# Performance work log

Hardware: AMD Instinct MI355X
Metric: run time of the kernel (lower is better)

The kernel has to match this reference:

```python
import jax, jax.numpy as jnp
import numpy as np

T, D, I, E, K = 2048, 1024, 1024, 8, 2  # tokens, dim, moe_inter_dim, n_experts, top_k


def setup_inputs() -> dict:
    key = jax.random.key(0)
    ks = jax.random.split(key, 6)
    x = jax.random.normal(ks[0], (T, D), dtype=jnp.float32)
    token_mask = jnp.ones((T,), dtype=bool)
    weights = jax.random.uniform(ks[1], (T, K), dtype=jnp.float32)
    indices = jax.random.randint(ks[2], (T, K), 0, E, dtype=jnp.int32)
    scale = 0.02
    gate_projs = jax.random.normal(ks[3], (E, I, D), dtype=jnp.float32) * scale
    up_projs = jax.random.normal(ks[4], (E, I, D), dtype=jnp.float32) * scale
    down_projs = jax.random.normal(ks[5], (E, D, I), dtype=jnp.float32) * scale
    return {"x": x, "token_mask": token_mask, "weights": weights,
            "indices": indices, "gate_projs": gate_projs,
            "up_projs": up_projs, "down_projs": down_projs}


def reference(x, token_mask, weights, indices, gate_projs, up_projs, down_projs):
    # Combined routing weight per (token, expert): sum over top-k slots that
    # selected expert e, zeroed for masked-out tokens. Equivalent to the
    # torch gather -> swiglu -> weighted scatter_add loop.
    n_experts = gate_projs.shape[0]
    one_hot = (indices[..., None] == jnp.arange(n_experts)).astype(x.dtype)  # [T,K,E]
    w = jnp.einsum('tk,tke->te', weights, one_hot)                            # [T,E]
    w = w * token_mask.astype(x.dtype)[:, None]
    # Per-expert SwiGLU over all tokens, combined with routing weights.
    g = jnp.einsum('td,eid->eti', x, gate_projs)   # [E,T,I]
    u = jnp.einsum('td,eid->eti', x, up_projs)     # [E,T,I]
    h = jax.nn.silu(g) * u                          # [E,T,I]
    out = jnp.einsum('eti,edi->etd', h, down_projs)  # [E,T,D]
    y = jnp.einsum('etd,te->td', out, w)             # [T,D]
    return y
```

## Files before the change

### kernel.cpp

```cpp
#include <hip/hip_runtime.h>
#include <hip/hip_bf16.h>

#define T_TOK 2048
#define DDIM  1024
#define IDIM  1024
#define NEXP  8
#define TOPK  2
#define MAXROWS (T_TOK * TOPK)

#define BM 64
#define BN 64
#define BK 32
#define LDT 40
#define BUFSZ (64 * LDT)

typedef __attribute__((ext_vector_type(8))) short          s16x8;
typedef __attribute__((ext_vector_type(8))) unsigned short u16x8;
typedef __attribute__((ext_vector_type(4))) float          f32x4;

__device__ __forceinline__ unsigned short f2bf(float f) {
    unsigned int u = __builtin_bit_cast(unsigned int, f);
    unsigned int r = 0x7fffu + ((u >> 16) & 1u);
    return (unsigned short)((u + r) >> 16);
}

__device__ __forceinline__ u16x8 pack8(const float4& a, const float4& b) {
    u16x8 v;
    v[0] = f2bf(a.x); v[1] = f2bf(a.y); v[2] = f2bf(a.z); v[3] = f2bf(a.w);
    v[4] = f2bf(b.x); v[5] = f2bf(b.y); v[6] = f2bf(b.z); v[7] = f2bf(b.w);
    return v;
}

__global__ void route_kernel(const int* __restrict__ indices,
                             const float* __restrict__ weights,
                             const void* __restrict__ mask,
                             int* __restrict__ counts, int* __restrict__ offsets,
                             int* __restrict__ tok, float* __restrict__ wslot) {
    __shared__ int cnt[NEXP], offs[NEXP], cur[NEXP];
    __shared__ int is_u8;
    const int tid = threadIdx.x;
    const unsigned char* m8  = (const unsigned char*)mask;
    const int*           m32 = (const int*)mask;
    if (tid < NEXP) cnt[tid] = 0;
    if (tid == 0) is_u8 = 0;
    __syncthreads();
    int found = 0;
    for (int i = tid; i < T_TOK; i += blockDim.x)
        if ((i & 3) != 0 && m8[i] != 0) found = 1;
    if (found) atomicOr(&is_u8, 1);
    __syncthreads();
    const int u8mode = is_u8;
    for (int idx = tid; idx < MAXROWS; idx += blockDim.x) {
        int t = idx >> 1;
        int active = u8mode ? (m8[t] != 0) : (m32[t] != 0);
        if (active) atomicAdd(&cnt[indices[idx]], 1);
    }
    __syncthreads();
    if (tid == 0) {
        int run = 0;
        for (int e = 0; e < NEXP; ++e) { offs[e] = run; run += cnt[e]; }
    }
    __syncthreads();
    if (tid < NEXP) { counts[tid] = cnt[tid]; offsets[tid] = offs[tid]; cur[tid] = offs[tid]; }
    __syncthreads();
    for (int idx = tid; idx < MAXROWS; idx += blockDim.x) {
        int t = idx >> 1;
        int active = u8mode ? (m8[t] != 0) : (m32[t] != 0);
        if (active) {
            int e = indices[idx];
            int p = atomicAdd(&cur[e], 1);
            tok[p]   = t;
            wslot[p] = weights[idx];
        }
    }
}

__global__ __launch_bounds__(256) void cvt_x_kernel(const float* __restrict__ x,
                                                    unsigned short* __restrict__ xb) {
    int i = (blockIdx.x * 256 + threadIdx.x) * 8;
    float4 a = *reinterpret_cast<const float4*>(x + i);
    float4 b = *reinterpret_cast<const float4*>(x + i + 4);
    *reinterpret_cast<u16x8*>(xb + i) = pack8(a, b);
}

__global__ __launch_bounds__(256) void gemm1_kernel(
    const unsigned short* __restrict__ xb,
    const float* __restrict__ gate, const float* __restrict__ up,
    const int* __restrict__ counts, const int* __restrict__ offsets,
    const int* __restrict__ tok, unsigned short* __restrict__ hb) {
    const int e     = blockIdx.z;
    const int n_e   = counts[e];
    const int tileM = blockIdx.y;
    if (tileM * BM >= n_e) return;
    const int off = offsets[e];
    const int n0  = blockIdx.x * BN;

    __shared__ unsigned short lA[2 * BUFSZ];
    __shared__ unsigned short lG[2 * BUFSZ];
    __shared__ unsigned short lU[2 * BUFSZ];

    const int tid  = threadIdx.x;
    const int lane = tid & 63;
    const int wid  = tid >> 6;
    const int wm   = wid >> 1, wn = wid & 1;

    const int sr = tid >> 2, sseg = tid & 3;
    const int rowIdx = tileM * BM + sr;
    const int tIdx = (rowIdx < n_e) ? tok[off + rowIdx] : tok[off];
    const unsigned short* aSrc = xb + (size_t)tIdx * DDIM + sseg * 8;
    const float* gSrc = gate + ((size_t)e * IDIM + n0 + sr) * DDIM + sseg * 8;
    const float* uSrc = up   + ((size_t)e * IDIM + n0 + sr) * DDIM + sseg * 8;
    const int dstOff = sr * LDT + sseg * 8;

    f32x4 accg[2][2] = {};
    f32x4 accu[2][2] = {};

    const int fr  = lane & 15;
    const int fkb = (lane >> 4) * 8;

    uint4  av;
    float4 gv0, gv1, uv0, uv1;

    auto LOAD = [&](int k0) {
        av  = *reinterpret_cast<const uint4*>(aSrc + k0);
        gv0 = *reinterpret_cast<const float4*>(gSrc + k0);
        gv1 = *reinterpret_cast<const float4*>(gSrc + k0 + 4);
        uv0 = *reinterpret_cast<const float4*>(uSrc + k0);
        uv1 = *reinterpret_cast<const float4*>(uSrc + k0 + 4);
    };

    auto STORE = [&](int b) {
        *reinterpret_cast<uint4*>(&lA[b * BUFSZ + dstOff]) = av;
        *reinterpret_cast<u16x8*>(&lG[b * BUFSZ + dstOff]) = pack8(gv0, gv1);
        *reinterpret_cast<u16x8*>(&lU[b * BUFSZ + dstOff]) = pack8(uv0, uv1);
    };

    auto COMPUTE = [&](int b) {
        const unsigned short* pA = &lA[b * BUFSZ];
        const unsigned short* pG = &lG[b * BUFSZ];
        const unsigned short* pU = &lU[b * BUFSZ];
        s16x8 a0  = *reinterpret_cast<const s16x8*>(pA + (wm * 32 + fr) * LDT + fkb);
        s16x8 a1  = *reinterpret_cast<const s16x8*>(pA + (wm * 32 + 16 + fr) * LDT + fkb);
        s16x8 bg0 = *reinterpret_cast<const s16x8*>(pG + (wn * 32 + fr) * LDT + fkb);
        s16x8 bg1 = *reinterpret_cast<const s16x8*>(pG + (wn * 32 + 16 + fr) * LDT + fkb);
        s16x8 bu0 = *reinterpret_cast<const s16x8*>(pU + (wn * 32 + fr) * LDT + fkb);
        s16x8 bu1 = *reinterpret_cast<const s16x8*>(pU + (wn * 32 + 16 + fr) * LDT + fkb);
        accg[0][0] = __builtin_amdgcn_mfma_f32_16x16x32_bf16(a0, bg0, accg[0][0], 0, 0, 0);
        accg[0][1] = __builtin_amdgcn_mfma_f32_16x16x32_bf16(a0, bg1, accg[0][1], 0, 0, 0);
        accg[1][0] = __builtin_amdgcn_mfma_f32_16x16x32_bf16(a1, bg0, accg[1][0], 0, 0, 0);
        accg[1][1] = __builtin_amdgcn_mfma_f32_16x16x32_bf16(a1, bg1, accg[1][1], 0, 0, 0);
        accu[0][0] = __builtin_amdgcn_mfma_f32_16x16x32_bf16(a0, bu0, accu[0][0], 0, 0, 0);
        accu[0][1] = __builtin_amdgcn_mfma_f32_16x16x32_bf16(a0, bu1, accu[0][1], 0, 0, 0);
        accu[1][0] = __builtin_amdgcn_mfma_f32_16x16x32_bf16(a1, bu0, accu[1][0], 0, 0, 0);
        accu[1][1] = __builtin_amdgcn_mfma_f32_16x16x32_bf16(a1, bu1, accu[1][1], 0, 0, 0);
    };

    LOAD(0);
    STORE(0);
    __syncthreads();
    const int NT = DDIM / BK;
    for (int t = 0; t < NT - 1; ++t) {
        LOAD((t + 1) * BK);
        COMPUTE(t & 1);
        STORE((t + 1) & 1);
        __syncthreads();
    }
    COMPUTE((NT - 1) & 1);

    const int rbase = tileM * BM;
#pragma unroll
    for (int m = 0; m < 2; ++m)
#pragma unroll
        for (int n = 0; n < 2; ++n)
#pragma unroll
            for (int j = 0; j < 4; ++j) {
                int rl = wm * 32 + m * 16 + (lane >> 4) * 4 + j;
                if (rbase + rl < n_e) {
                    int col = wn * 32 + n * 16 + fr;
                    float g = accg[m][n][j];
                    float u = accu[m][n][j];
                    float h = (g / (1.0f + __expf(-g))) * u;
                    hb[(size_t)(off + rbase + rl) * IDIM + n0 + col] = f2bf(h);
                }
            }
}

__global__ __launch_bounds__(256) void gemm2_kernel(
    const unsigned short* __restrict__ hb, const float* __restrict__ down,
    const int* __restrict__ counts, const int* __restrict__ offsets,
    const int* __restrict__ tok, const float* __restrict__ wslot,
    float* __restrict__ y) {
    const int e     = blockIdx.z;
    const int n_e   = counts[e];
    const int tileM = blockIdx.y;
    if (tileM * BM >= n_e) return;
    const int off = offsets[e];
    const int n0  = blockIdx.x * BN;

    __shared__ unsigned short lA[2 * BUFSZ];
    __shared__ unsigned short lB[2 * BUFSZ];

    const int tid  = threadIdx.x;
    const int lane = tid & 63;
    const int wid  = tid >> 6;
    const int wm   = wid >> 1, wn = wid & 1;

    const int sr = tid >> 2, sseg = tid & 3;
    const int rowIdx = tileM * BM + sr;
    const int hrow = (rowIdx < n_e) ? (off + rowIdx) : off;
    const unsigned short* aSrc = hb + (size_t)hrow * IDIM + sseg * 8;
    const float* bSrc = down + ((size_t)e * DDIM + n0 + sr) * IDIM + sseg * 8;
    const int dstOff = sr * LDT + sseg * 8;

    f32x4 acc[2][2] = {};

    const int fr  = lane & 15;
    const int fkb = (lane >> 4) * 8;

    uint4  av;
    float4 bv0, bv1;

    auto LOAD = [&](int k0) {
        av  = *reinterpret_cast<const uint4*>(aSrc + k0);
        bv0 = *reinterpret_cast<const float4*>(bSrc + k0);
        bv1 = *reinterpret_cast<const float4*>(bSrc + k0 + 4);
    };

    auto STORE = [&](int b) {
        *reinterpret_cast<uint4*>(&lA[b * BUFSZ + dstOff]) = av;
        *reinterpret_cast<u16x8*>(&lB[b * BUFSZ + dstOff]) = pack8(bv0, bv1);
    };

    auto COMPUTE = [&](int b) {
        const unsigned short* pA = &lA[b * BUFSZ];
        const unsigned short* pB = &lB[b * BUFSZ];
        s16x8 a0 = *reinterpret_cast<const s16x8*>(pA + (wm * 32 + fr) * LDT + fkb);
        s16x8 a1 = *reinterpret_cast<const s16x8*>(pA + (wm * 32 + 16 + fr) * LDT + fkb);
        s16x8 b0 = *reinterpret_cast<const s16x8*>(pB + (wn * 32 + fr) * LDT + fkb);
        s16x8 b1 = *reinterpret_cast<const s16x8*>(pB + (wn * 32 + 16 + fr) * LDT + fkb);
        acc[0][0] = __builtin_amdgcn_mfma_f32_16x16x32_bf16(a0, b0, acc[0][0], 0, 0, 0);
        acc[0][1] = __builtin_amdgcn_mfma_f32_16x16x32_bf16(a0, b1, acc[0][1], 0, 0, 0);
        acc[1][0] = __builtin_amdgcn_mfma_f32_16x16x32_bf16(a1, b0, acc[1][0], 0, 0, 0);
        acc[1][1] = __builtin_amdgcn_mfma_f32_16x16x32_bf16(a1, b1, acc[1][1], 0, 0, 0);
    };

    LOAD(0);
    STORE(0);
    __syncthreads();
    const int NT = IDIM / BK;
    for (int t = 0; t < NT - 1; ++t) {
        LOAD((t + 1) * BK);
        COMPUTE(t & 1);
        STORE((t + 1) & 1);
        __syncthreads();
    }
    COMPUTE((NT - 1) & 1);

    const int rbase = tileM * BM;
#pragma unroll
    for (int m = 0; m < 2; ++m)
#pragma unroll
        for (int n = 0; n < 2; ++n)
#pragma unroll
            for (int j = 0; j < 4; ++j) {
                int rl = wm * 32 + m * 16 + (lane >> 4) * 4 + j;
                if (rbase + rl < n_e) {
                    int col = wn * 32 + n * 16 + fr;
                    int row = off + rbase + rl;
                    float v = acc[m][n][j] * wslot[row];
                    atomicAdd(&y[(size_t)tok[row] * DDIM + n0 + col], v);
                }
            }
}

extern "C" void kernel_launch(void* const* d_in, const int* in_sizes, int n_in,
                              void* d_out, int out_size, void* d_ws, size_t ws_size,
                              hipStream_t stream) {
    const float* x       = (const float*)d_in[0];
    const void*  mask    = d_in[1];
    const float* weights = (const float*)d_in[2];
    const int*   indices = (const int*)d_in[3];
    const float* gate    = (const float*)d_in[4];
    const float* up      = (const float*)d_in[5];
    const float* down    = (const float*)d_in[6];
    float*       y       = (float*)d_out;

    char* ws = (char*)d_ws;
    int*            counts  = (int*)ws;
    int*            offsets = (int*)(ws + 32);
    int*            tok     = (int*)(ws + 256);
    float*          wslot   = (float*)(ws + 256 + MAXROWS * 4);
    unsigned short* xb      = (unsigned short*)(ws + 65536);
    unsigned short* hb      = (unsigned short*)(ws + 65536 + (size_t)T_TOK * DDIM * 2);

    hipMemsetAsync(d_out, 0, (size_t)out_size * sizeof(float), stream);
    route_kernel<<<1, 256, 0, stream>>>(indices, weights, mask, counts, offsets, tok, wslot);
    cvt_x_kernel<<<(T_TOK * DDIM / 8) / 256, 256, 0, stream>>>(x, xb);

    dim3 g1(IDIM / BN, MAXROWS / BM, NEXP);
    gemm1_kernel<<<g1, 256, 0, stream>>>(xb, gate, up, counts, offsets, tok, hb);
    dim3 g2(DDIM / BN, MAXROWS / BM, NEXP);
    gemm2_kernel<<<g2, 256, 0, stream>>>(hb, down, counts, offsets, tok, wslot, y);
}
```

Baseline: 129.8 us.

## Deepen register prefetch to two K-tiles in both MoE GEMM kernels

Both grouped GEMM kernels now keep two sets of prefetch registers, so global loads for tile t+2 are issued before computing tile t, with the loop unrolled by two. This lengthens the window for hiding global-load latency behind MFMA work. The float-to-bf16 conversion is also switched to the HIP intrinsic. The cost is higher register pressure from the doubled staging registers, which can lower occupancy.

```diff
diff --git a/kernel.cpp b/kernel.cpp
--- a/kernel.cpp
+++ b/kernel.cpp
@@ -19,9 +19,7 @@
 typedef __attribute__((ext_vector_type(4))) float          f32x4;
 
 __device__ __forceinline__ unsigned short f2bf(float f) {
-    unsigned int u = __builtin_bit_cast(unsigned int, f);
-    unsigned int r = 0x7fffu + ((u >> 16) & 1u);
-    return (unsigned short)((u + r) >> 16);
+    return __builtin_bit_cast(unsigned short, __float2bfloat16(f));
 }
 
 __device__ __forceinline__ u16x8 pack8(const float4& a, const float4& b) {
@@ -118,22 +116,25 @@
     const int fr  = lane & 15;
     const int fkb = (lane >> 4) * 8;
 
-    uint4  av;
-    float4 gv0, gv1, uv0, uv1;
-
-    auto LOAD = [&](int k0) {
-        av  = *reinterpret_cast<const uint4*>(aSrc + k0);
-        gv0 = *reinterpret_cast<const float4*>(gSrc + k0);
-        gv1 = *reinterpret_cast<const float4*>(gSrc + k0 + 4);
-        uv0 = *reinterpret_cast<const float4*>(uSrc + k0);
-        uv1 = *reinterpret_cast<const float4*>(uSrc + k0 + 4);
-    };
-
-    auto STORE = [&](int b) {
-        *reinterpret_cast<uint4*>(&lA[b * BUFSZ + dstOff]) = av;
-        *reinterpret_cast<u16x8*>(&lG[b * BUFSZ + dstOff]) = pack8(gv0, gv1);
-        *reinterpret_cast<u16x8*>(&lU[b * BUFSZ + dstOff]) = pack8(uv0, uv1);
-    };
+    uint4  av0, av1;
+    float4 g0a, g0b, u0a, u0b;
+    float4 g1a, g1b, u1a, u1b;
+
+#define G1_LOAD(AV, GA, GB, UA, UB, K0)                                   \
+    do {                                                                  \
+        AV = *reinterpret_cast<const uint4*>(aSrc + (K0));                \
+        GA = *reinterpret_cast<const float4*>(gSrc + (K0));               \
+        GB = *reinterpret_cast<const float4*>(gSrc + (K0) + 4);           \
+        UA = *reinterpret_cast<const float4*>(uSrc + (K0));               \
+        UB = *reinterpret_cast<const float4*>(uSrc + (K0) + 4);           \
+    } while (0)
+
+#define G1_STORE(AV, GA, GB, UA, UB, B)                                   \
+    do {                                                                  \
+        *reinterpret_cast<uint4*>(&lA[(B) * BUFSZ + dstOff]) = AV;        \
+        *reinterpret_cast<u16x8*>(&lG[(B) * BUFSZ + dstOff]) = pack8(GA, GB); \
+        *reinterpret_cast<u16x8*>(&lU[(B) * BUFSZ + dstOff]) = pack8(UA, UB); \
+    } while (0)
 
     auto COMPUTE = [&](int b) {
         const unsigned short* pA = &lA[b * BUFSZ];
@@ -155,17 +156,27 @@
         accu[1][1] = __builtin_amdgcn_mfma_f32_16x16x32_bf16(a1, bu1, accu[1][1], 0, 0, 0);
     };
 
-    LOAD(0);
-    STORE(0);
-    __syncthreads();
     const int NT = DDIM / BK;
-    for (int t = 0; t < NT - 1; ++t) {
-        LOAD((t + 1) * BK);
-        COMPUTE(t & 1);
-        STORE((t + 1) & 1);
+    G1_LOAD(av0, g0a, g0b, u0a, u0b, 0);
+    G1_STORE(av0, g0a, g0b, u0a, u0b, 0);
+    G1_LOAD(av1, g1a, g1b, u1a, u1b, BK);
+    __syncthreads();
+    for (int t = 0; t + 3 < NT; t += 2) {
+        G1_LOAD(av0, g0a, g0b, u0a, u0b, (t + 2) * BK);
+        COMPUTE(0);
+        G1_STORE(av1, g1a, g1b, u1a, u1b, 1);
         __syncthreads();
-    }
-    COMPUTE((NT - 1) & 1);
+        G1_LOAD(av1, g1a, g1b, u1a, u1b, (t + 3) * BK);
+        COMPUTE(1);
+        G1_STORE(av0, g0a, g0b, u0a, u0b, 0);
+        __syncthreads();
+    }
+    COMPUTE(0);
+    G1_STORE(av1, g1a, g1b, u1a, u1b, 1);
+    __syncthreads();
+    COMPUTE(1);
+#undef G1_LOAD
+#undef G1_STORE
 
     const int rbase = tileM * BM;
 #pragma unroll
@@ -217,19 +228,21 @@
     const int fr  = lane & 15;
     const int fkb = (lane >> 4) * 8;
 
-    uint4  av;
-    float4 bv0, bv1;
-
-    auto LOAD = [&](int k0) {
-        av  = *reinterpret_cast<const uint4*>(aSrc + k0);
-        bv0 = *reinterpret_cast<const float4*>(bSrc + k0);
-        bv1 = *reinterpret_cast<const float4*>(bSrc + k0 + 4);
-    };
-
-    auto STORE = [&](int b) {
-        *reinterpret_cast<uint4*>(&lA[b * BUFSZ + dstOff]) = av;
-        *reinterpret_cast<u16x8*>(&lB[b * BUFSZ + dstOff]) = pack8(bv0, bv1);
-    };
+    uint4  av0, av1;
+    float4 b0a, b0b, b1a, b1b;
+
+#define G2_LOAD(AV, BA, BB, K0)                                           \
+    do {                                                                  \
+        AV = *reinterpret_cast<const uint4*>(aSrc + (K0));                \
+        BA = *reinterpret_cast<const float4*>(bSrc + (K0));               \
+        BB = *reinterpret_cast<const float4*>(bSrc + (K0) + 4);           \
+    } while (0)
+
+#define G2_STORE(AV, BA, BB, B)                                           \
+    do {                                                                  \
+        *reinterpret_cast<uint4*>(&lA[(B) * BUFSZ + dstOff]) = AV;        \
+        *reinterpret_cast<u16x8*>(&lB[(B) * BUFSZ + dstOff]) = pack8(BA, BB); \
+    } while (0)
 
     auto COMPUTE = [&](int b) {
         const unsigned short* pA = &lA[b * BUFSZ];
@@ -244,17 +257,27 @@
         acc[1][1] = __builtin_amdgcn_mfma_f32_16x16x32_bf16(a1, b1, acc[1][1], 0, 0, 0);
     };
 
-    LOAD(0);
-    STORE(0);
-    __syncthreads();
     const int NT = IDIM / BK;
-    for (int t = 0; t < NT - 1; ++t) {
-        LOAD((t + 1) * BK);
-        COMPUTE(t & 1);
-        STORE((t + 1) & 1);
+    G2_LOAD(av0, b0a, b0b, 0);
+    G2_STORE(av0, b0a, b0b, 0);
+    G2_LOAD(av1, b1a, b1b, BK);
+    __syncthreads();
+    for (int t = 0; t + 3 < NT; t += 2) {
+        G2_LOAD(av0, b0a, b0b, (t + 2) * BK);
+        COMPUTE(0);
+        G2_STORE(av1, b1a, b1b, 1);
         __syncthreads();
-    }
-    COMPUTE((NT - 1) & 1);
+        G2_LOAD(av1, b1a, b1b, (t + 3) * BK);
+        COMPUTE(1);
+        G2_STORE(av0, b0a, b0b, 0);
+        __syncthreads();
+    }
+    COMPUTE(0);
+    G2_STORE(av1, b1a, b1b, 1);
+    __syncthreads();
+    COMPUTE(1);
+#undef G2_LOAD
+#undef G2_STORE
 
     const int rbase = tileM * BM;
 #pragma unroll
```

After: 127.2 us. 1.02x faster.

## Stage GEMM tiles via direct global-to-LDS loads with XOR-swizzled layout

Applied to the files above, without the earlier changes.

Both expert GEMM kernels now copy tiles straight from global memory into LDS with global_load_lds 16-byte transfers, replacing the register round trip. Weights are kept as fp32 in LDS and converted to bf16 when read as MFMA fragments, and an XOR swizzle replaces row padding to avoid bank conflicts. This cuts register pressure and VALU work in the staging path, but fp32 weight tiles double the LDS footprint. Each conversion now runs once per reading wave, so it is repeated redundantly. The bf16 conversion also switches to the library intrinsic.

```diff
diff --git a/kernel.cpp b/kernel.cpp
--- a/kernel.cpp
+++ b/kernel.cpp
@@ -11,17 +11,13 @@
 #define BM 64
 #define BN 64
 #define BK 32
-#define LDT 40
-#define BUFSZ (64 * LDT)
 
 typedef __attribute__((ext_vector_type(8))) short          s16x8;
 typedef __attribute__((ext_vector_type(8))) unsigned short u16x8;
 typedef __attribute__((ext_vector_type(4))) float          f32x4;
 
 __device__ __forceinline__ unsigned short f2bf(float f) {
-    unsigned int u = __builtin_bit_cast(unsigned int, f);
-    unsigned int r = 0x7fffu + ((u >> 16) & 1u);
-    return (unsigned short)((u + r) >> 16);
+    return __builtin_bit_cast(unsigned short, __float2bfloat16(f));
 }
 
 __device__ __forceinline__ u16x8 pack8(const float4& a, const float4& b) {
@@ -29,6 +25,16 @@
     v[0] = f2bf(a.x); v[1] = f2bf(a.y); v[2] = f2bf(a.z); v[3] = f2bf(a.w);
     v[4] = f2bf(b.x); v[5] = f2bf(b.y); v[6] = f2bf(b.z); v[7] = f2bf(b.w);
     return v;
+}
+
+__device__ __forceinline__ s16x8 cvt8(const float4& a, const float4& b) {
+    return __builtin_bit_cast(s16x8, pack8(a, b));
+}
+
+__device__ __forceinline__ void gll16(const void* g, void* l) {
+    __builtin_amdgcn_global_load_lds(
+        (const __attribute__((address_space(1))) void*)g,
+        (__attribute__((address_space(3))) void*)l, 16, 0, 0);
 }
 
 __global__ void route_kernel(const int* __restrict__ indices,
@@ -83,6 +89,7 @@
     *reinterpret_cast<u16x8*>(xb + i) = pack8(a, b);
 }
 
+
 __global__ __launch_bounds__(256) void gemm1_kernel(
     const unsigned short* __restrict__ xb,
     const float* __restrict__ gate, const float* __restrict__ up,
@@ -95,74 +102,82 @@
     const int off = offsets[e];
     const int n0  = blockIdx.x * BN;
 
-    __shared__ unsigned short lA[2 * BUFSZ];
-    __shared__ unsigned short lG[2 * BUFSZ];
-    __shared__ unsigned short lU[2 * BUFSZ];
+    __shared__ unsigned short lA[2][2048];
+    __shared__ float          lG[2][2048];
+    __shared__ float          lU[2][2048];
 
     const int tid  = threadIdx.x;
     const int lane = tid & 63;
     const int wid  = tid >> 6;
     const int wm   = wid >> 1, wn = wid & 1;
 
-    const int sr = tid >> 2, sseg = tid & 3;
-    const int rowIdx = tileM * BM + sr;
-    const int tIdx = (rowIdx < n_e) ? tok[off + rowIdx] : tok[off];
-    const unsigned short* aSrc = xb + (size_t)tIdx * DDIM + sseg * 8;
-    const float* gSrc = gate + ((size_t)e * IDIM + n0 + sr) * DDIM + sseg * 8;
-    const float* uSrc = up   + ((size_t)e * IDIM + n0 + sr) * DDIM + sseg * 8;
-    const int dstOff = sr * LDT + sseg * 8;
+    const int rA  = wid * 8 + (lane >> 3);
+    const int ilA = (lane & 7) ^ (rA & 7);
+    const int trA = 2 * rA + (ilA & 1);
+    {   }
+    const int rowIdxA = tileM * BM + trA;
+    const int tIdxA = (rowIdxA < n_e) ? tok[off + rowIdxA] : tok[off];
+    const unsigned short* aSrc = xb + (size_t)tIdxA * DDIM + (ilA >> 1) * 8;
+    const int rB0 = (2 * wid) * 8 + (lane >> 3);
+    const int rB1 = rB0 + 8;
+    const int ilB0 = (lane & 7) ^ (rB0 & 7);
+    const int ilB1 = (lane & 7) ^ (rB1 & 7);
+    const float* gSrc0 = gate + ((size_t)e * IDIM + n0 + rB0) * DDIM + ilB0 * 4;
+    const float* gSrc1 = gate + ((size_t)e * IDIM + n0 + rB1) * DDIM + ilB1 * 4;
+    const float* uSrc0 = up   + ((size_t)e * IDIM + n0 + rB0) * DDIM + ilB0 * 4;
+    const float* uSrc1 = up   + ((size_t)e * IDIM + n0 + rB1) * DDIM + ilB1 * 4;
 
     f32x4 accg[2][2] = {};
     f32x4 accu[2][2] = {};
 
-    const int fr  = lane & 15;
-    const int fkb = (lane >> 4) * 8;
-
-    uint4  av;
-    float4 gv0, gv1, uv0, uv1;
-
-    auto LOAD = [&](int k0) {
-        av  = *reinterpret_cast<const uint4*>(aSrc + k0);
-        gv0 = *reinterpret_cast<const float4*>(gSrc + k0);
-        gv1 = *reinterpret_cast<const float4*>(gSrc + k0 + 4);
-        uv0 = *reinterpret_cast<const float4*>(uSrc + k0);
-        uv1 = *reinterpret_cast<const float4*>(uSrc + k0 + 4);
+    const int fr = lane & 15;
+    const int s8 = lane >> 4;
+
+    auto STAGE = [&](int b, int t) {
+        const int k0 = t * BK;
+        gll16(aSrc  + k0, &lA[b][wid * 512]);
+        gll16(gSrc0 + k0, &lG[b][(2 * wid) * 256]);
+        gll16(gSrc1 + k0, &lG[b][(2 * wid + 1) * 256]);
+        gll16(uSrc0 + k0, &lU[b][(2 * wid) * 256]);
+        gll16(uSrc1 + k0, &lU[b][(2 * wid + 1) * 256]);
     };
 
-    auto STORE = [&](int b) {
-        *reinterpret_cast<uint4*>(&lA[b * BUFSZ + dstOff]) = av;
-        *reinterpret_cast<u16x8*>(&lG[b * BUFSZ + dstOff]) = pack8(gv0, gv1);
-        *reinterpret_cast<u16x8*>(&lU[b * BUFSZ + dstOff]) = pack8(uv0, uv1);
+    auto COMPUTE = [&](int b) {
+        s16x8 a[2];
+#pragma unroll
+        for (int m = 0; m < 2; ++m) {
+            int trow = wm * 32 + m * 16 + fr;
+            int r = trow >> 1, p = trow & 1;
+            int is_ = (2 * s8 + p) ^ (r & 7);
+            a[m] = *reinterpret_cast<const s16x8*>(&lA[b][r * 64 + is_ * 8]);
+        }
+        s16x8 bg[2], bu[2];
+#pragma unroll
+        for (int nf = 0; nf < 2; ++nf) {
+            int n = wn * 32 + nf * 16 + fr;
+            int xr = n & 7;
+            float4 g0 = *reinterpret_cast<const float4*>(&lG[b][n * 32 + ((2 * s8) ^ xr) * 4]);
+            float4 g1 = *reinterpret_cast<const float4*>(&lG[b][n * 32 + ((2 * s8 + 1) ^ xr) * 4]);
+            float4 u0 = *reinterpret_cast<const float4*>(&lU[b][n * 32 + ((2 * s8) ^ xr) * 4]);
+            float4 u1 = *reinterpret_cast<const float4*>(&lU[b][n * 32 + ((2 * s8 + 1) ^ xr) * 4]);
+            bg[nf] = cvt8(g0, g1);
+            bu[nf] = cvt8(u0, u1);
+        }
+#pragma unroll
+        for (int m = 0; m < 2; ++m)
+#pragma unroll
+            for (int nf = 0; nf < 2; ++nf) {
+                accg[m][nf] = __builtin_amdgcn_mfma_f32_16x16x32_bf16(a[m], bg[nf], accg[m][nf], 0, 0, 0);
+                accu[m][nf] = __builtin_amdgcn_mfma_f32_16x16x32_bf16(a[m], bu[nf], accu[m][nf], 0, 0, 0);
+            }
     };
 
-    auto COMPUTE = [&](int b) {
-        const unsigned short* pA = &lA[b * BUFSZ];
-        const unsigned short* pG = &lG[b * BUFSZ];
-        const unsigned short* pU = &lU[b * BUFSZ];
-        s16x8 a0  = *reinterpret_cast<const s16x8*>(pA + (wm * 32 + fr) * LDT + fkb);
-        s16x8 a1  = *reinterpret_cast<const s16x8*>(pA + (wm * 32 + 16 + fr) * LDT + fkb);
-        s16x8 bg0 = *reinterpret_cast<const s16x8*>(pG + (wn * 32 + fr) * LDT + fkb);
-        s16x8 bg1 = *reinterpret_cast<const s16x8*>(pG + (wn * 32 + 16 + fr) * LDT + fkb);
-        s16x8 bu0 = *reinterpret_cast<const s16x8*>(pU + (wn * 32 + fr) * LDT + fkb);
-        s16x8 bu1 = *reinterpret_cast<const s16x8*>(pU + (wn * 32 + 16 + fr) * LDT + fkb);
-        accg[0][0] = __builtin_amdgcn_mfma_f32_16x16x32_bf16(a0, bg0, accg[0][0], 0, 0, 0);
-        accg[0][1] = __builtin_amdgcn_mfma_f32_16x16x32_bf16(a0, bg1, accg[0][1], 0, 0, 0);
-        accg[1][0] = __builtin_amdgcn_mfma_f32_16x16x32_bf16(a1, bg0, accg[1][0], 0, 0, 0);
-        accg[1][1] = __builtin_amdgcn_mfma_f32_16x16x32_bf16(a1, bg1, accg[1][1], 0, 0, 0);
-        accu[0][0] = __builtin_amdgcn_mfma_f32_16x16x32_bf16(a0, bu0, accu[0][0], 0, 0, 0);
-        accu[0][1] = __builtin_amdgcn_mfma_f32_16x16x32_bf16(a0, bu1, accu[0][1], 0, 0, 0);
-        accu[1][0] = __builtin_amdgcn_mfma_f32_16x16x32_bf16(a1, bu0, accu[1][0], 0, 0, 0);
-        accu[1][1] = __builtin_amdgcn_mfma_f32_16x16x32_bf16(a1, bu1, accu[1][1], 0, 0, 0);
-    };
-
-    LOAD(0);
-    STORE(0);
-    __syncthreads();
     const int NT = DDIM / BK;
+    STAGE(0, 0);
+    __syncthreads();
     for (int t = 0; t < NT - 1; ++t) {
-        LOAD((t + 1) * BK);
+        STAGE((t + 1) & 1, t + 1);
         COMPUTE(t & 1);
-        STORE((t + 1) & 1);
         __syncthreads();
     }
     COMPUTE((NT - 1) & 1);
@@ -197,61 +212,70 @@
     const int off = offsets[e];
     const int n0  = blockIdx.x * BN;
 
-    __shared__ unsigned short lA[2 * BUFSZ];
-    __shared__ unsigned short lB[2 * BUFSZ];
+    __shared__ unsigned short lA[2][2048];
+    __shared__ float          lB[2][2048];
 
     const int tid  = threadIdx.x;
     const int lane = tid & 63;
     const int wid  = tid >> 6;
     const int wm   = wid >> 1, wn = wid & 1;
 
-    const int sr = tid >> 2, sseg = tid & 3;
-    const int rowIdx = tileM * BM + sr;
-    const int hrow = (rowIdx < n_e) ? (off + rowIdx) : off;
-    const unsigned short* aSrc = hb + (size_t)hrow * IDIM + sseg * 8;
-    const float* bSrc = down + ((size_t)e * DDIM + n0 + sr) * IDIM + sseg * 8;
-    const int dstOff = sr * LDT + sseg * 8;
+    const int rA  = wid * 8 + (lane >> 3);
+    const int ilA = (lane & 7) ^ (rA & 7);
+    const int trA = 2 * rA + (ilA & 1);
+    const int rowIdxA = tileM * BM + trA;
+    const int hrowA = (rowIdxA < n_e) ? (off + rowIdxA) : off;
+    const unsigned short* aSrc = hb + (size_t)hrowA * IDIM + (ilA >> 1) * 8;
+    const int rB0 = (2 * wid) * 8 + (lane >> 3);
+    const int rB1 = rB0 + 8;
+    const int ilB0 = (lane & 7) ^ (rB0 & 7);
+    const int ilB1 = (lane & 7) ^ (rB1 & 7);
+    const float* bSrc0 = down + ((size_t)e * DDIM + n0 + rB0) * IDIM + ilB0 * 4;
+    const float* bSrc1 = down + ((size_t)e * DDIM + n0 + rB1) * IDIM + ilB1 * 4;
 
     f32x4 acc[2][2] = {};
 
-    const int fr  = lane & 15;
-    const int fkb = (lane >> 4) * 8;
-
-    uint4  av;
-    float4 bv0, bv1;
-
-    auto LOAD = [&](int k0) {
-        av  = *reinterpret_cast<const uint4*>(aSrc + k0);
-        bv0 = *reinterpret_cast<const float4*>(bSrc + k0);
-        bv1 = *reinterpret_cast<const float4*>(bSrc + k0 + 4);
+    const int fr = lane & 15;
+    const int s8 = lane >> 4;
+
+    auto STAGE = [&](int b, int t) {
+        const int k0 = t * BK;
+        gll16(aSrc  + k0, &lA[b][wid * 512]);
+        gll16(bSrc0 + k0, &lB[b][(2 * wid) * 256]);
+        gll16(bSrc1 + k0, &lB[b][(2 * wid + 1) * 256]);
     };
 
-    auto STORE = [&](int b) {
-        *reinterpret_cast<uint4*>(&lA[b * BUFSZ + dstOff]) = av;
-        *reinterpret_cast<u16x8*>(&lB[b * BUFSZ + dstOff]) = pack8(bv0, bv1);
+    auto COMPUTE = [&](int b) {
+        s16x8 a[2];
+#pragma unroll
+        for (int m = 0; m < 2; ++m) {
+            int trow = wm * 32 + m * 16 + fr;
+            int r = trow >> 1, p = trow & 1;
+            int is_ = (2 * s8 + p) ^ (r & 7);
+            a[m] = *reinterpret_cast<const s16x8*>(&lA[b][r * 64 + is_ * 8]);
+        }
+        s16x8 bf[2];
+#pragma unroll
+        for (int nf = 0; nf < 2; ++nf) {
+            int n = wn * 32 + nf * 16 + fr;
+            int xr = n & 7;
+            float4 b0 = *reinterpret_cast<const float4*>(&lB[b][n * 32 + ((2 * s8) ^ xr) * 4]);
+            float4 b1 = *reinterpret_cast<const float4*>(&lB[b][n * 32 + ((2 * s8 + 1) ^ xr) * 4]);
+            bf[nf] = cvt8(b0, b1);
+        }
+#pragma unroll
+        for (int m = 0; m < 2; ++m)
+#pragma unroll
+            for (int nf = 0; nf < 2; ++nf)
+                acc[m][nf] = __builtin_amdgcn_mfma_f32_16x16x32_bf16(a[m], bf[nf], acc[m][nf], 0, 0, 0);
     };
 
-    auto COMPUTE = [&](int b) {
-        const unsigned short* pA = &lA[b * BUFSZ];
-        const unsigned short* pB = &lB[b * BUFSZ];
-        s16x8 a0 = *reinterpret_cast<const s16x8*>(pA + (wm * 32 + fr) * LDT + fkb);
-        s16x8 a1 = *reinterpret_cast<const s16x8*>(pA + (wm * 32 + 16 + fr) * LDT + fkb);
-        s16x8 b0 = *reinterpret_cast<const s16x8*>(pB + (wn * 32 + fr) * LDT + fkb);
-        s16x8 b1 = *reinterpret_cast<const s16x8*>(pB + (wn * 32 + 16 + fr) * LDT + fkb);
-        acc[0][0] = __builtin_amdgcn_mfma_f32_16x16x32_bf16(a0, b0, acc[0][0], 0, 0, 0);
-        acc[0][1] = __builtin_amdgcn_mfma_f32_16x16x32_bf16(a0, b1, acc[0][1], 0, 0, 0);
-        acc[1][0] = __builtin_amdgcn_mfma_f32_16x16x32_bf16(a1, b0, acc[1][0], 0, 0, 0);
-        acc[1][1] = __builtin_amdgcn_mfma_f32_16x16x32_bf16(a1, b1, acc[1][1], 0, 0, 0);
-    };
-
-    LOAD(0);
-    STORE(0);
-    __syncthreads();
     const int NT = IDIM / BK;
+    STAGE(0, 0);
+    __syncthreads();
     for (int t = 0; t < NT - 1; ++t) {
-        LOAD((t + 1) * BK);
+        STAGE((t + 1) & 1, t + 1);
         COMPUTE(t & 1);
-        STORE((t + 1) & 1);
         __syncthreads();
     }
     COMPUTE((NT - 1) & 1);
```

Result: slower. 135.7 us (+4.5%).
